# Kernel tuning notes

Measured on AMD Instinct MI355X. Metric: run time of the kernel, lower is better.

The kernel has to match this reference:

```python
import jax, jax.numpy as jnp
import numpy as np

B, F, W, H, D = 128, 1024, 32, 64, 64  # batch, n_features, window_size, hidden_state, output_dim


def setup_inputs() -> dict:
    key = jax.random.key(0)
    ks = jax.random.split(key, 8)
    sd = 0.05
    return {
        "x": jax.random.normal(ks[0], (B, F, W), jnp.float32),
        # dense_state: Dense(output_dim) on concat([cell, hidden]) -> [2H, D]
        "W_state": jax.random.normal(ks[1], (2 * H, D), jnp.float32) * sd,
        "b_state": jnp.zeros((D,), jnp.float32),
        # dense: Dense(output_dim, use_bias=False) on input last dim W -> [W, D]
        "W_in": jax.random.normal(ks[2], (W, D), jnp.float32) * sd,
        # Dense(1) scoring layer (shared; original re-creates it each call)
        "w_attn": jax.random.normal(ks[3], (D, 1), jnp.float32) * sd,
        "b_attn": jnp.zeros((1,), jnp.float32),
        # Keras LSTMCell params, gate order i, f, g(c~), o
        "Wx": jax.random.normal(ks[4], (F, 4 * H), jnp.float32) * sd,
        "Wh": jax.random.normal(ks[5], (H, 4 * H), jnp.float32) * sd,
        "b_lstm": jnp.zeros((4 * H,), jnp.float32),
    }


def _forward(x, W_state, b_state, W_in, w_attn, b_attn, Wx, Wh, b_lstm):
    b, f, w = x.shape
    h_dim = Wh.shape[0]
    # dense(input) is loop-invariant: [B, F, D]
    dense_in = jnp.einsum('bfw,wd->bfd', x, W_in)
    xs = jnp.moveaxis(x, 2, 0)  # [W, B, F]: per-timestep slices input[:, :, i]
    h0 = jnp.zeros((b, h_dim), x.dtype)
    c0 = jnp.zeros((b, h_dim), x.dtype)

    def step(carry, x_t):
        h, c = carry
        # original unpacks `s, h = state` with state=[h,c], so it concats [cell, hidden]
        attn_in = jnp.concatenate([c, h], axis=1)             # [B, 2H]
        z = jnp.tanh(attn_in @ W_state + b_state)[:, None, :] + dense_in  # [B, F, D]
        presoft = z @ w_attn + b_attn                         # [B, F, 1]
        # faithful: softmax over last (size-1) axis -> all ones
        alpha = jax.nn.softmax(presoft, axis=-1)
        x_tilde = alpha[..., 0] * x_t                         # [B, F]
        gates = x_tilde @ Wx + h @ Wh + b_lstm                # [B, 4H]
        i_g, f_g, g_g, o_g = jnp.split(gates, 4, axis=1)
        c_new = jax.nn.sigmoid(f_g) * c + jax.nn.sigmoid(i_g) * jnp.tanh(g_g)
        h_new = jax.nn.sigmoid(o_g) * jnp.tanh(c_new)
        # original appends state[1] == CELL state (due to the s,h swap)
        return (h_new, c_new), c_new

    _, outs = jax.lax.scan(step, (h0, c0), xs)                # [W, B, H]
    return jnp.transpose(outs, (1, 0, 2))                     # [B, W, H]


def reference(x, W_state, b_state, W_in, w_attn, b_attn, Wx, Wh, b_lstm):
    return _forward(x, W_state, b_state, W_in, w_attn, b_attn, Wx, Wh, b_lstm)
```

## Files before the change

kernel.cpp:

```cpp
#include <hip/hip_runtime.h>
#include <math.h>

#define B_   128
#define F_   1024
#define W_   32
#define H_   64
#define K4H  256
#define M_   (B_ * W_)
#define K2_  (2 * F_)

typedef __attribute__((ext_vector_type(8))) short  short8;
typedef __attribute__((ext_vector_type(4))) float  f32x4;

__device__ __forceinline__ unsigned bf16_rne(float v) {
  unsigned u = __float_as_uint(v);
  return (u + 0x7FFFu + ((u >> 16) & 1u)) >> 16;
}
__device__ __forceinline__ unsigned pack_hilo(float v) {
  unsigned hi = bf16_rne(v);
  float    hf = __uint_as_float(hi << 16);
  unsigned lo = bf16_rne(v - hf);
  return hi | (lo << 16);
}

__global__ __launch_bounds__(256) void conv_w(const float* __restrict__ Wx,
                                              unsigned* __restrict__ B2) {
  __shared__ unsigned T[256][17];
  const int tid = threadIdx.x;
  const int f0  = blockIdx.x * 16;
#pragma unroll
  for (int i = 0; i < 4; ++i) {
    int l = tid + i * 256;
    int n0 = (l & 63) * 4;
    int fl = l >> 6;
    float4 v = *(const float4*)&Wx[(size_t)(f0 + fl) * K4H + n0];
    T[n0 + 0][fl] = pack_hilo(v.x);
    T[n0 + 1][fl] = pack_hilo(v.y);
    T[n0 + 2][fl] = pack_hilo(v.z);
    T[n0 + 3][fl] = pack_hilo(v.w);
  }
  __syncthreads();
#pragma unroll
  for (int i = 0; i < 4; ++i) {
    int l  = tid + i * 256;
    int c4 = (l & 3) * 4;
    int n  = l >> 2;
    uint4 o;
    o.x = T[n][c4 + 0]; o.y = T[n][c4 + 1]; o.z = T[n][c4 + 2]; o.w = T[n][c4 + 3];
    *(uint4*)&B2[(size_t)n * (K2_ / 2) + f0 + c4] = o;
  }
}

template <int S>
__global__ __launch_bounds__(256, 1) void gemm_mfma(
    const float* __restrict__ x,
    const unsigned* __restrict__ B2,
    float* __restrict__ Gp) {
  constexpr int NIT = 32 / S;
  __shared__ unsigned lA[128 * 36];
  __shared__ unsigned lB[128 * 36];
  const int tid   = threadIdx.x;
  const int mtile = blockIdx.x;
  const int ntile = blockIdx.y;
  const int s     = blockIdx.z;
  const int wv = tid >> 6, lane = tid & 63;
  const int wm = wv & 1, wn = wv >> 1;
  const int lm = lane & 15, q = lane >> 4;

  f32x4 acc[4][4];
#pragma unroll
  for (int a = 0; a < 4; ++a)
#pragma unroll
    for (int bb = 0; bb < 4; ++bb) acc[a][bb] = (f32x4){0.f, 0.f, 0.f, 0.f};

  const int b0 = mtile * 4;
  float4 ax[4];
  uint4  bxr[4];

  auto prefetch = [&](int iter) {
    const int f0 = (s * NIT + iter) * 32;
#pragma unroll
    for (int i = 0; i < 4; ++i) {
      int l  = tid + i * 256;
      int t0 = (l & 7) * 4;
      int fl = (l >> 3) & 31;
      int bl = l >> 8;
      ax[i] = *(const float4*)&x[(((size_t)(b0 + bl)) * F_ + (f0 + fl)) * W_ + t0];
    }
#pragma unroll
    for (int i = 0; i < 4; ++i) {
      int l   = tid + i * 256;
      int c16 = l & 7;
      int nl  = l >> 3;
      bxr[i] = *(const uint4*)&B2[(size_t)(ntile * 128 + nl) * (K2_ / 2) + f0 + c16 * 4];
    }
  };

  prefetch(0);
  const int jx = (tid >> 3) & 3;
  for (int iter = 0; iter < NIT; ++iter) {
    __syncthreads();
#pragma unroll
    for (int i = 0; i < 4; ++i) {
      int l  = tid + i * 256;
      int t0 = (l & 7) * 4;
      int fl = (l >> 3) & 31;
      int bl = l >> 8;
      int m0 = bl * 32 + t0;
      float vals[4] = {ax[i].x, ax[i].y, ax[i].z, ax[i].w};
#pragma unroll
      for (int j = 0; j < 4; ++j) {
        int jj = j ^ jx;
        lA[(m0 + jj) * 36 + fl] = pack_hilo(vals[jj]);
      }
    }
#pragma unroll
    for (int i = 0; i < 4; ++i) {
      int l   = tid + i * 256;
      int c16 = l & 7;
      int nl  = l >> 3;
      *(uint4*)&lB[nl * 36 + c16 * 4] = bxr[i];
    }
    __syncthreads();
    if (iter + 1 < NIT) prefetch(iter + 1);
#pragma unroll
    for (int step = 0; step < 2; ++step) {
      short8 aF[4], bF[4];
#pragma unroll
      for (int mt = 0; mt < 4; ++mt) {
        int row = wm * 64 + mt * 16 + lm;
        aF[mt] = *(const short8*)&lA[row * 36 + step * 16 + q * 4];
      }
#pragma unroll
      for (int nt = 0; nt < 4; ++nt) {
        int row = wn * 64 + nt * 16 + lm;
        bF[nt] = *(const short8*)&lB[row * 36 + step * 16 + q * 4];
      }
#pragma unroll
      for (int mt = 0; mt < 4; ++mt)
#pragma unroll
        for (int nt = 0; nt < 4; ++nt)
          acc[mt][nt] = __builtin_amdgcn_mfma_f32_16x16x32_bf16(
              aF[mt], bF[nt], acc[mt][nt], 0, 0, 0);
    }
  }
  float* Gs = Gp + (size_t)s * ((size_t)M_ * K4H);
#pragma unroll
  for (int mt = 0; mt < 4; ++mt)
#pragma unroll
    for (int nt = 0; nt < 4; ++nt)
#pragma unroll
      for (int r = 0; r < 4; ++r) {
        int m = mtile * 128 + wm * 64 + mt * 16 + q * 4 + r;
        int n = ntile * 128 + wn * 64 + nt * 16 + lm;
        Gs[(size_t)m * K4H + n] = acc[mt][nt][r];
      }
}

__device__ __forceinline__ float bcastlane(float v, int l) {
  return __uint_as_float(__builtin_amdgcn_readlane(__float_as_uint(v), l));
}
__device__ __forceinline__ float sigm(float v)   { return 1.f / (1.f + __expf(-v)); }
__device__ __forceinline__ float tanh_f(float v) { return 1.f - 2.f / (__expf(2.f * v) + 1.f); }

template <int S>
__global__ __launch_bounds__(256, 1) void lstm_seq(
    const float* __restrict__ Gp, const float* __restrict__ Wh,
    const float* __restrict__ bl, float* __restrict__ out) {
  __shared__ float sact[2][4][64];
  const int b = blockIdx.x, tid = threadIdx.x;
  const int w = tid >> 6, u = tid & 63;
  const int k = w * 64 + u;

  float wc[64];
#pragma unroll
  for (int j = 0; j < 64; ++j) wc[j] = Wh[j * K4H + k];
  const float bk = bl[k];
  const size_t base = (size_t)b * W_ * K4H + k;
  const size_t sstr = (size_t)M_ * K4H;

  float h = 0.f, c = 0.f;
  float p = 0.f;
#pragma unroll
  for (int ss = 0; ss < S; ++ss) p += Gp[ss * sstr + base];

  for (int t = 0; t < W_; ++t) {
    float nx = 0.f;
    if (t + 1 < W_) {
#pragma unroll
      for (int ss = 0; ss < S; ++ss)
        nx += Gp[ss * sstr + base + (size_t)(t + 1) * K4H];
    }
    float a0 = p + bk, a1 = 0.f, a2 = 0.f, a3 = 0.f;
#pragma unroll
    for (int j = 0; j < 64; j += 4) {
      a0 = fmaf(bcastlane(h, j),     wc[j],     a0);
      a1 = fmaf(bcastlane(h, j + 1), wc[j + 1], a1);
      a2 = fmaf(bcastlane(h, j + 2), wc[j + 2], a2);
      a3 = fmaf(bcastlane(h, j + 3), wc[j + 3], a3);
    }
    float g = (a0 + a1) + (a2 + a3);
    float act = (w == 2) ? tanh_f(g) : sigm(g);
    sact[t & 1][w][u] = act;
    __syncthreads();
    float si = sact[t & 1][0][u];
    float sf = sact[t & 1][1][u];
    float tg = sact[t & 1][2][u];
    float so = sact[t & 1][3][u];
    c = fmaf(sf, c, si * tg);
    h = so * tanh_f(c);
    if (w == 0) out[((size_t)b * W_ + t) * H_ + u] = c;
    p = nx;
  }
}

extern "C" void kernel_launch(void* const* d_in, const int* in_sizes, int n_in,
                              void* d_out, int out_size, void* d_ws, size_t ws_size,
                              hipStream_t stream) {
  const float* x      = (const float*)d_in[0];
  const float* Wx     = (const float*)d_in[6];
  const float* Wh     = (const float*)d_in[7];
  const float* b_lstm = (const float*)d_in[8];
  float* out = (float*)d_out;

  const size_t gbytes = (size_t)M_ * K4H * sizeof(float);

  if (ws_size >= 4 * gbytes + (1u << 20)) {
    float*    Gp = (float*)d_ws;
    unsigned* B2 = (unsigned*)((char*)d_ws + 4 * gbytes);
    conv_w      <<<dim3(64),       dim3(256), 0, stream>>>(Wx, B2);
    gemm_mfma<4><<<dim3(32, 2, 4), dim3(256), 0, stream>>>(x, B2, Gp);
    lstm_seq<4> <<<dim3(B_),       dim3(256), 0, stream>>>(Gp, Wh, b_lstm, out);
  } else if (ws_size >= 2 * gbytes + (1u << 20)) {
    float*    Gp = (float*)d_ws;
    unsigned* B2 = (unsigned*)((char*)d_ws + 2 * gbytes);
    conv_w      <<<dim3(64),       dim3(256), 0, stream>>>(Wx, B2);
    gemm_mfma<2><<<dim3(32, 2, 2), dim3(256), 0, stream>>>(x, B2, Gp);
    lstm_seq<2> <<<dim3(B_),       dim3(256), 0, stream>>>(Gp, Wh, b_lstm, out);
  } else {
    float*    Gp = (float*)d_ws;
    unsigned* B2 = (unsigned*)((char*)d_ws + gbytes);
    conv_w      <<<dim3(64),       dim3(256), 0, stream>>>(Wx, B2);
    gemm_mfma<1><<<dim3(32, 2, 1), dim3(256), 0, stream>>>(x, B2, Gp);
    lstm_seq<1> <<<dim3(B_),       dim3(256), 0, stream>>>(Gp, Wh, b_lstm, out);
  }
}
```

Measured before the change: 121.3 us.

## Fuse Wx bf16 conversion into GEMM and deepen LSTM gate prefetch

Drops the separate conv_w kernel that converted and transposed Wx into hi/lo bf16 pairs. The GEMM now loads fp32 Wx directly and packs it into shared memory with transposed scalar stores. This removes one launch and a workspace round trip, but repeats the conversion in every GEMM block and may add LDS bank conflicts. The A-tile XOR swizzle is also removed, and the LSTM kernel now prefetches gate partials two timesteps ahead instead of one.

```diff
diff --git a/kernel.cpp b/kernel.cpp
--- a/kernel.cpp
+++ b/kernel.cpp
@@ -23,38 +23,10 @@
   return hi | (lo << 16);
 }
 
-__global__ __launch_bounds__(256) void conv_w(const float* __restrict__ Wx,
-                                              unsigned* __restrict__ B2) {
-  __shared__ unsigned T[256][17];
-  const int tid = threadIdx.x;
-  const int f0  = blockIdx.x * 16;
-#pragma unroll
-  for (int i = 0; i < 4; ++i) {
-    int l = tid + i * 256;
-    int n0 = (l & 63) * 4;
-    int fl = l >> 6;
-    float4 v = *(const float4*)&Wx[(size_t)(f0 + fl) * K4H + n0];
-    T[n0 + 0][fl] = pack_hilo(v.x);
-    T[n0 + 1][fl] = pack_hilo(v.y);
-    T[n0 + 2][fl] = pack_hilo(v.z);
-    T[n0 + 3][fl] = pack_hilo(v.w);
-  }
-  __syncthreads();
-#pragma unroll
-  for (int i = 0; i < 4; ++i) {
-    int l  = tid + i * 256;
-    int c4 = (l & 3) * 4;
-    int n  = l >> 2;
-    uint4 o;
-    o.x = T[n][c4 + 0]; o.y = T[n][c4 + 1]; o.z = T[n][c4 + 2]; o.w = T[n][c4 + 3];
-    *(uint4*)&B2[(size_t)n * (K2_ / 2) + f0 + c4] = o;
-  }
-}
-
 template <int S>
 __global__ __launch_bounds__(256, 1) void gemm_mfma(
     const float* __restrict__ x,
-    const unsigned* __restrict__ B2,
+    const float* __restrict__ Wx,
     float* __restrict__ Gp) {
   constexpr int NIT = 32 / S;
   __shared__ unsigned lA[128 * 36];
@@ -75,7 +47,7 @@
 
   const int b0 = mtile * 4;
   float4 ax[4];
-  uint4  bxr[4];
+  float4 bx[4];
 
   auto prefetch = [&](int iter) {
     const int f0 = (s * NIT + iter) * 32;
@@ -89,15 +61,14 @@
     }
 #pragma unroll
     for (int i = 0; i < 4; ++i) {
-      int l   = tid + i * 256;
-      int c16 = l & 7;
-      int nl  = l >> 3;
-      bxr[i] = *(const uint4*)&B2[(size_t)(ntile * 128 + nl) * (K2_ / 2) + f0 + c16 * 4];
+      int l    = tid + i * 256;
+      int col4 = l & 31;
+      int fl   = l >> 5;
+      bx[i] = *(const float4*)&Wx[(size_t)(f0 + fl) * K4H + ntile * 128 + col4 * 4];
     }
   };
 
   prefetch(0);
-  const int jx = (tid >> 3) & 3;
   for (int iter = 0; iter < NIT; ++iter) {
     __syncthreads();
 #pragma unroll
@@ -107,19 +78,21 @@
       int fl = (l >> 3) & 31;
       int bl = l >> 8;
       int m0 = bl * 32 + t0;
-      float vals[4] = {ax[i].x, ax[i].y, ax[i].z, ax[i].w};
-#pragma unroll
-      for (int j = 0; j < 4; ++j) {
-        int jj = j ^ jx;
-        lA[(m0 + jj) * 36 + fl] = pack_hilo(vals[jj]);
-      }
-    }
-#pragma unroll
-    for (int i = 0; i < 4; ++i) {
-      int l   = tid + i * 256;
-      int c16 = l & 7;
-      int nl  = l >> 3;
-      *(uint4*)&lB[nl * 36 + c16 * 4] = bxr[i];
+      lA[(m0 + 0) * 36 + fl] = pack_hilo(ax[i].x);
+      lA[(m0 + 1) * 36 + fl] = pack_hilo(ax[i].y);
+      lA[(m0 + 2) * 36 + fl] = pack_hilo(ax[i].z);
+      lA[(m0 + 3) * 36 + fl] = pack_hilo(ax[i].w);
+    }
+#pragma unroll
+    for (int i = 0; i < 4; ++i) {
+      int l    = tid + i * 256;
+      int col4 = l & 31;
+      int fl   = l >> 5;
+      int n0   = col4 * 4;
+      lB[(n0 + 0) * 36 + fl] = pack_hilo(bx[i].x);
+      lB[(n0 + 1) * 36 + fl] = pack_hilo(bx[i].y);
+      lB[(n0 + 2) * 36 + fl] = pack_hilo(bx[i].z);
+      lB[(n0 + 3) * 36 + fl] = pack_hilo(bx[i].w);
     }
     __syncthreads();
     if (iter + 1 < NIT) prefetch(iter + 1);
@@ -180,18 +153,22 @@
   const size_t sstr = (size_t)M_ * K4H;
 
   float h = 0.f, c = 0.f;
-  float p = 0.f;
-#pragma unroll
-  for (int ss = 0; ss < S; ++ss) p += Gp[ss * sstr + base];
+  float pv[S], n1[S];
+#pragma unroll
+  for (int ss = 0; ss < S; ++ss) {
+    pv[ss] = Gp[ss * sstr + base];
+    n1[ss] = Gp[ss * sstr + base + K4H];
+  }
 
   for (int t = 0; t < W_; ++t) {
-    float nx = 0.f;
-    if (t + 1 < W_) {
-#pragma unroll
-      for (int ss = 0; ss < S; ++ss)
-        nx += Gp[ss * sstr + base + (size_t)(t + 1) * K4H];
-    }
-    float a0 = p + bk, a1 = 0.f, a2 = 0.f, a3 = 0.f;
+    float n2[S];
+#pragma unroll
+    for (int ss = 0; ss < S; ++ss)
+      n2[ss] = (t + 2 < W_) ? Gp[ss * sstr + base + (size_t)(t + 2) * K4H] : 0.f;
+
+    float a0 = bk, a1 = 0.f, a2 = 0.f, a3 = 0.f;
+#pragma unroll
+    for (int ss = 0; ss < S; ++ss) a0 += pv[ss];
 #pragma unroll
     for (int j = 0; j < 64; j += 4) {
       a0 = fmaf(bcastlane(h, j),     wc[j],     a0);
@@ -210,7 +187,8 @@
     c = fmaf(sf, c, si * tg);
     h = so * tanh_f(c);
     if (w == 0) out[((size_t)b * W_ + t) * H_ + u] = c;
-    p = nx;
+#pragma unroll
+    for (int ss = 0; ss < S; ++ss) { pv[ss] = n1[ss]; n1[ss] = n2[ss]; }
   }
 }
 
@@ -222,26 +200,18 @@
   const float* Wh     = (const float*)d_in[7];
   const float* b_lstm = (const float*)d_in[8];
   float* out = (float*)d_out;
+  float* Gp  = (float*)d_ws;
 
   const size_t gbytes = (size_t)M_ * K4H * sizeof(float);
 
-  if (ws_size >= 4 * gbytes + (1u << 20)) {
-    float*    Gp = (float*)d_ws;
-    unsigned* B2 = (unsigned*)((char*)d_ws + 4 * gbytes);
-    conv_w      <<<dim3(64),       dim3(256), 0, stream>>>(Wx, B2);
-    gemm_mfma<4><<<dim3(32, 2, 4), dim3(256), 0, stream>>>(x, B2, Gp);
+  if (ws_size >= 4 * gbytes) {
+    gemm_mfma<4><<<dim3(32, 2, 4), dim3(256), 0, stream>>>(x, Wx, Gp);
     lstm_seq<4> <<<dim3(B_),       dim3(256), 0, stream>>>(Gp, Wh, b_lstm, out);
-  } else if (ws_size >= 2 * gbytes + (1u << 20)) {
-    float*    Gp = (float*)d_ws;
-    unsigned* B2 = (unsigned*)((char*)d_ws + 2 * gbytes);
-    conv_w      <<<dim3(64),       dim3(256), 0, stream>>>(Wx, B2);
-    gemm_mfma<2><<<dim3(32, 2, 2), dim3(256), 0, stream>>>(x, B2, Gp);
+  } else if (ws_size >= 2 * gbytes) {
+    gemm_mfma<2><<<dim3(32, 2, 2), dim3(256), 0, stream>>>(x, Wx, Gp);
     lstm_seq<2> <<<dim3(B_),       dim3(256), 0, stream>>>(Gp, Wh, b_lstm, out);
   } else {
-    float*    Gp = (float*)d_ws;
-    unsigned* B2 = (unsigned*)((char*)d_ws + gbytes);
-    conv_w      <<<dim3(64),       dim3(256), 0, stream>>>(Wx, B2);
-    gemm_mfma<1><<<dim3(32, 2, 1), dim3(256), 0, stream>>>(x, B2, Gp);
+    gemm_mfma<1><<<dim3(32, 2, 1), dim3(256), 0, stream>>>(x, Wx, Gp);
     lstm_seq<1> <<<dim3(B_),       dim3(256), 0, stream>>>(Gp, Wh, b_lstm, out);
   }
 }
```

Measured after the change: 126.3 us. 1.04x slower.
